# Kernel tuning notes

Hardware: AMD Instinct MI355X
Metric: run time of the kernel (lower is better)

The kernel has to match this reference:

```python
import jax, jax.numpy as jnp
import numpy as np

T = 200                      # TRAIN_ROIS_PER_IMAGE
RATIO = 0.33                 # ROI_POSITIVE_RATIO
P_MAX = int(T * RATIO)       # max positive ROIs (66)
MH, MW = 28, 28              # MASK_SHAPE
STD = jnp.array([0.1, 0.1, 0.2, 0.2], jnp.float32)  # BBOX_STD_DEV
EPS = 1e-6


def _iou(a, b):
    # a [N,4], b [G,4] -> [N,G] IoU (same math as overlaps_graph, without tiling)
    ay1, ax1, ay2, ax2 = a[:, 0:1], a[:, 1:2], a[:, 2:3], a[:, 3:4]
    by1, bx1, by2, bx2 = b[None, :, 0], b[None, :, 1], b[None, :, 2], b[None, :, 3]
    iy = jnp.maximum(jnp.minimum(ay2, by2) - jnp.maximum(ay1, by1), 0.0)
    ix = jnp.maximum(jnp.minimum(ax2, bx2) - jnp.maximum(ax1, bx1), 0.0)
    inter = iy * ix
    union = (ay2 - ay1) * (ax2 - ax1) + (by2 - by1) * (bx2 - bx1) - inter
    return inter / jnp.maximum(union, EPS)


def _box_refinement(box, gt):
    # standard Mask R-CNN box_refinement_graph
    h = jnp.maximum(box[:, 2] - box[:, 0], EPS)
    w = jnp.maximum(box[:, 3] - box[:, 1], EPS)
    cy = box[:, 0] + 0.5 * h
    cx = box[:, 1] + 0.5 * w
    gh = jnp.maximum(gt[:, 2] - gt[:, 0], EPS)
    gw = jnp.maximum(gt[:, 3] - gt[:, 1], EPS)
    gcy = gt[:, 0] + 0.5 * gh
    gcx = gt[:, 1] + 0.5 * gw
    return jnp.stack([(gcy - cy) / h, (gcx - cx) / w,
                      jnp.log(gh / h), jnp.log(gw / w)], axis=-1)


def _crop_and_resize(imgs, boxes):
    # imgs [T,H,W], boxes [T,4] normalized; TF crop_and_resize bilinear semantics,
    # extrapolation_value = 0 for samples outside [0, H-1] x [0, W-1].
    Tn, H, W = imgs.shape
    y1, x1, y2, x2 = boxes[:, 0], boxes[:, 1], boxes[:, 2], boxes[:, 3]
    iy = jnp.arange(MH, dtype=jnp.float32)
    ix = jnp.arange(MW, dtype=jnp.float32)
    ys = y1[:, None] * (H - 1) + iy[None, :] * ((y2 - y1) * (H - 1) / (MH - 1))[:, None]  # [T,MH]
    xs = x1[:, None] * (W - 1) + ix[None, :] * ((x2 - x1) * (W - 1) / (MW - 1))[:, None]  # [T,MW]
    y0 = jnp.floor(ys); x0 = jnp.floor(xs)
    wy = (ys - y0)[:, :, None]
    wx = (xs - x0)[:, None, :]
    y0i = jnp.clip(y0, 0, H - 1).astype(jnp.int32)
    y1i = jnp.clip(y0 + 1, 0, H - 1).astype(jnp.int32)
    x0i = jnp.clip(x0, 0, W - 1).astype(jnp.int32)
    x1i = jnp.clip(x0 + 1, 0, W - 1).astype(jnp.int32)
    t = jnp.arange(Tn)[:, None, None]
    v00 = imgs[t, y0i[:, :, None], x0i[:, None, :]]
    v01 = imgs[t, y0i[:, :, None], x1i[:, None, :]]
    v10 = imgs[t, y1i[:, :, None], x0i[:, None, :]]
    v11 = imgs[t, y1i[:, :, None], x1i[:, None, :]]
    val = (v00 * (1 - wx) + v01 * wx) * (1 - wy) + (v10 * (1 - wx) + v11 * wx) * wy
    ok = ((ys >= 0) & (ys <= H - 1))[:, :, None] & ((xs >= 0) & (xs <= W - 1))[:, None, :]
    return jnp.where(ok, val, 0.0)


def _targets_one(proposals, class_ids, boxes, masks):
    # proposals [N,4], class_ids [G] int, boxes [G,4], masks [H,W,G]
    N = proposals.shape[0]
    # zero-padding trim expressed as validity masks (jit-friendly fixed shapes)
    valid_prop = jnp.any(proposals != 0, axis=1)
    valid_gt = jnp.any(boxes != 0, axis=1)
    non_crowd = (class_ids > 0) & valid_gt
    crowd = (class_ids < 0) & valid_gt

    ov = _iou(proposals, boxes)                              # [N,G]
    ov_nc = jnp.where(non_crowd[None, :], ov, -1.0)          # mask crowd/padded gt
    roi_iou_max = ov_nc.max(axis=1)
    crowd_max = jnp.where(crowd[None, :], ov, 0.0).max(axis=1)

    pos_mask = valid_prop & (roi_iou_max >= 0.5)
    neg_mask = valid_prop & (roi_iou_max < 0.5) & (crowd_max < 0.001)

    # deterministic selection (original uses tf.random.shuffle): positives first-in-order
    pos_order = jnp.argsort(jnp.where(pos_mask, 0, 1))
    neg_order = jnp.argsort(jnp.where(neg_mask, 0, 1))
    pos_count = jnp.minimum(pos_mask.sum(), P_MAX)
    neg_needed = jnp.floor(pos_count.astype(jnp.float32) / RATIO).astype(jnp.int32) - pos_count
    neg_count = jnp.minimum(jnp.minimum(neg_needed, neg_mask.sum()), T - pos_count)

    slot = jnp.arange(T)
    is_pos = slot < pos_count
    is_neg = (slot >= pos_count) & (slot < pos_count + neg_count)
    src = jnp.where(is_pos,
                    pos_order[jnp.clip(slot, 0, N - 1)],
                    neg_order[jnp.clip(slot - pos_count, 0, N - 1)])
    rois = jnp.where((is_pos | is_neg)[:, None], proposals[src], 0.0)

    assign = jnp.argmax(ov_nc[src], axis=1)                  # gt assignment per slot
    gt_box = boxes[assign]
    gt_cls = jnp.where(is_pos, class_ids[assign], 0)

    deltas = _box_refinement(rois, gt_box) / STD
    deltas = jnp.where(is_pos[:, None], deltas, 0.0)

    # USE_MINI_MASK: roi box in gt-box-normalized coordinates
    gy1, gx1, gy2, gx2 = gt_box[:, 0], gt_box[:, 1], gt_box[:, 2], gt_box[:, 3]
    gh = jnp.maximum(gy2 - gy1, EPS)
    gw = jnp.maximum(gx2 - gx1, EPS)
    mm = jnp.stack([(rois[:, 0] - gy1) / gh, (rois[:, 1] - gx1) / gw,
                    (rois[:, 2] - gy1) / gh, (rois[:, 3] - gx1) / gw], axis=-1)

    roi_masks = jnp.moveaxis(jnp.take(masks, assign, axis=2), 2, 0)  # [T,H,W]
    m = jnp.round(_crop_and_resize(roi_masks, mm))
    m = jnp.where(is_pos[:, None, None], m, 0.0)
    return rois, gt_cls, deltas, m


def setup_inputs() -> dict:
    key = jax.random.key(0)
    ks = jax.random.split(key, 4)
    B, N, G, HM = 16, 2000, 200, 56

    def boxes_of(k, shape):
        k1, k2, k3, k4 = jax.random.split(k, 4)
        y1 = jax.random.uniform(k1, shape) * 0.5
        x1 = jax.random.uniform(k2, shape) * 0.5
        h = 0.1 + jax.random.uniform(k3, shape) * 0.4
        w = 0.1 + jax.random.uniform(k4, shape) * 0.4
        return jnp.stack([y1, x1, y1 + h, x1 + w], axis=-1)

    proposals = boxes_of(ks[0], (B, N))
    proposals = proposals * (jnp.arange(N) < N - 200)[None, :, None]  # zero-padded tail
    prior_class_ids = jax.random.randint(ks[1], (B, G), -1, 81).astype(jnp.int32)  # -1=crowd, 0=padding
    prior_boxes = boxes_of(ks[2], (B, G)) * (prior_class_ids != 0)[..., None]
    prior_masks = (jax.random.uniform(ks[3], (B, HM, HM, G)) > 0.5).astype(jnp.float32)
    return {"proposals": proposals, "prior_class_ids": prior_class_ids,
            "prior_boxes": prior_boxes, "prior_masks": prior_masks}


def reference(proposals, prior_class_ids, prior_boxes, prior_masks):
    rois, cls, deltas, masks = jax.vmap(_targets_one)(proposals, prior_class_ids,
                                                      prior_boxes, prior_masks)
    return rois, cls, deltas, masks
```

## Files before the change

### kernel.cpp

```cpp
#include <hip/hip_runtime.h>
#include <math.h>

#pragma clang fp contract(off)

#define BN    16
#define NP    2000
#define NG    200
#define NT    200
#define PMAX  66
#define EPSF  1e-6f
#define MH    28
#define MW    28
#define HM    56
#define NPIX  (HM*HM)
#define NW    49
#define NGP   256
#define NPW   32

#define KA_BLOCKS 128
#define KG_BLOCKS (49*4*BN)

__global__ __launch_bounds__(256) void kF(
    const float* __restrict__ proposals, const int* __restrict__ cls_ids,
    const float* __restrict__ boxes, const float* __restrict__ masks,
    unsigned long long* __restrict__ selbits, int* __restrict__ assign_ws,
    unsigned long long* __restrict__ bits)
{
#pragma clang fp contract(off)
  const int tid  = threadIdx.x;
  const int lane = tid & 63;
  const int wv   = tid >> 6;

  __shared__ float4 gbox[NG];
  __shared__ float  garea[NG];
  __shared__ int    gflag[NG];
  __shared__ unsigned long long sw[64];

  if (blockIdx.x < KA_BLOCKS) {
    const int b = blockIdx.x >> 3;
    const int bxa = blockIdx.x & 7;

    for (int j = tid; j < NG; j += 256) {
      float4 g = reinterpret_cast<const float4*>(boxes + (size_t)b * NG * 4)[j];
      int c = cls_ids[b * NG + j];
      bool vg = (g.x != 0.f) || (g.y != 0.f) || (g.z != 0.f) || (g.w != 0.f);
      gbox[j]  = g;
      garea[j] = (g.z - g.x) * (g.w - g.y);
      gflag[j] = vg ? (c > 0 ? 1 : (c < 0 ? 2 : 0)) : 0;
    }
    __syncthreads();

    const int i  = bxa * 256 + tid;
    const bool act = (i < NP);
    const int ic = act ? i : (NP - 1);

    float4 p = reinterpret_cast<const float4*>(proposals + (size_t)b * NP * 4)[ic];
    bool vp = act && ((p.x != 0.f) || (p.y != 0.f) || (p.z != 0.f) || (p.w != 0.f));
    float pa = (p.z - p.x) * (p.w - p.y);

    float best = -3.0e38f;
    int   bestj = 0;
    float cmax = 0.f;
    for (int j = 0; j < NG; ++j) {
      float4 g = gbox[j];
      float iy = fmaxf(fminf(p.z, g.z) - fmaxf(p.x, g.x), 0.f);
      float ix = fmaxf(fminf(p.w, g.w) - fmaxf(p.y, g.y), 0.f);
      float inter = iy * ix;
      float uni = (pa + garea[j]) - inter;
      float iou = inter / fmaxf(uni, EPSF);
      int fl = gflag[j];
      float v = (fl == 1) ? iou : -1.0f;
      if (v > best) { best = v; bestj = j; }
      if (fl == 2) cmax = fmaxf(cmax, iou);
    }
    bool pos = vp && (best >= 0.5f);
    bool neg = vp && (best < 0.5f) && (cmax < 0.001f);
    unsigned long long bp = __ballot(pos);
    unsigned long long bn = __ballot(neg);
    if (lane == 0) {
      int w = bxa * 4 + wv;
      selbits[(size_t)b * 64 + w]       = bp;
      selbits[(size_t)b * 64 + 32 + w]  = bn;
    }
    if (act) assign_ws[b * NP + i] = bestj;
  } else {
    int idx = blockIdx.x - KA_BLOCKS;
    const int pword = idx % 49;
    idx /= 49;
    const int gw0 = (idx & 3) * 64;
    const int b   = idx >> 2;
    const int p0  = pword * 64;

    const bool gok = (gw0 + lane) < NG;
    const float* mbase = masks + (size_t)b * NPIX * NG + gw0 + lane;
    for (int e = 0; e < 16; ++e) {
      int pl = e * 4 + wv;
      float v = 0.f;
      if (gok) v = mbase[(size_t)(p0 + pl) * NG];
      unsigned long long word = __ballot(v != 0.f);
      if (lane == 0) sw[pl] = word;
    }
    __syncthreads();

    unsigned long long w0 = sw[lane];
    for (int k = 0; k < 16; ++k) {
      int gl = wv * 16 + k;
      unsigned long long word = __ballot((int)((w0 >> gl) & 1ULL));
      if (lane == 0 && (gw0 + gl) < NG)
        bits[(size_t)(b * NGP + gw0 + gl) * NW + pword] = word;
    }
  }
}

__global__ __launch_bounds__(256) void kS(
    const float* __restrict__ proposals, const int* __restrict__ cls_ids,
    const float* __restrict__ boxes, const int* __restrict__ assign_ws,
    const unsigned long long* __restrict__ selbits,
    const unsigned long long* __restrict__ bits, float* __restrict__ out)
{
#pragma clang fp contract(off)
  const int s = blockIdx.x;
  const int b = s / NT;
  const int t = s - b * NT;
  const int q = threadIdx.x;

  __shared__ unsigned long long sel[64];
  __shared__ unsigned long long pb[NW];

  if (q < 64) sel[q] = selbits[(size_t)b * 64 + q];
  __syncthreads();

  int pos_total = 0, neg_total = 0;
  for (int w = 0; w < NPW; ++w) {
    pos_total += __popcll(sel[w]);
    neg_total += __popcll(sel[32 + w]);
  }
  int pos_count = min(pos_total, PMAX);
  int neg_needed = (int)floorf((float)pos_count / 0.33f) - pos_count;
  int neg_count = min(min(neg_needed, neg_total), NT - pos_count);

  const bool ispos = (t < pos_count);
  const bool isneg = (!ispos) && (t < pos_count + neg_count);

  float r0 = 0.f, r1 = 0.f, r2 = 0.f, r3 = 0.f;
  float d0 = 0.f, d1 = 0.f, d2 = 0.f, d3 = 0.f;
  float m0 = 0.f, m1 = 0.f, m2 = 0.f, m3 = 0.f;
  float clsf = 0.f;
  int a = -1;

  if (ispos || isneg) {
    int k = ispos ? t : (t - pos_count);
    const int base = ispos ? 0 : 32;
    int i = 0;
    for (int w = 0; w < NPW; ++w) {
      unsigned long long word = sel[base + w];
      int c = __popcll(word);
      if (k < c) {
        for (int r = 0; r < k; ++r) word &= word - 1ULL;
        i = w * 64 + __builtin_ctzll(word);
        break;
      }
      k -= c;
    }
    float4 p = reinterpret_cast<const float4*>(proposals + (size_t)b * NP * 4)[i];
    r0 = p.x; r1 = p.y; r2 = p.z; r3 = p.w;
    if (ispos) {
      a = assign_ws[b * NP + i];
      float4 g = reinterpret_cast<const float4*>(boxes + (size_t)b * NG * 4)[a];
      float h  = fmaxf(r2 - r0, EPSF);
      float w  = fmaxf(r3 - r1, EPSF);
      float cy = r0 + 0.5f * h;
      float cx = r1 + 0.5f * w;
      float gh = fmaxf(g.z - g.x, EPSF);
      float gw = fmaxf(g.w - g.y, EPSF);
      float gcy = g.x + 0.5f * gh;
      float gcx = g.y + 0.5f * gw;
      d0 = ((gcy - cy) / h) / 0.1f;
      d1 = ((gcx - cx) / w) / 0.1f;
      d2 = logf(gh / h) / 0.2f;
      d3 = logf(gw / w) / 0.2f;
      m0 = (r0 - g.x) / gh;
      m1 = (r1 - g.y) / gw;
      m2 = (r2 - g.x) / gh;
      m3 = (r3 - g.y) / gw;
      clsf = (float)cls_ids[b * NG + a];
    }
  }

  if (q == 0) {
    float* rois = out;
    float* cls  = out + BN * NT * 4;
    float* dlt  = out + BN * NT * 4 + BN * NT;
    rois[s * 4 + 0] = r0; rois[s * 4 + 1] = r1;
    rois[s * 4 + 2] = r2; rois[s * 4 + 3] = r3;
    cls[s] = clsf;
    dlt[s * 4 + 0] = d0; dlt[s * 4 + 1] = d1;
    dlt[s * 4 + 2] = d2; dlt[s * 4 + 3] = d3;
  }

  float4* om = reinterpret_cast<float4*>(
      out + (size_t)(BN * NT * 9) + (size_t)s * (MH * MW));
  if (!ispos) {
    if (q < (MH * MW) / 4) om[q] = make_float4(0.f, 0.f, 0.f, 0.f);
    return;
  }

  if (q < NW) pb[q] = bits[(size_t)(b * NGP + a) * NW + q];
  __syncthreads();
  if (q >= (MH * MW) / 4) return;

  float sy = (m2 - m0) * 55.0f / 27.0f;
  float sx = (m3 - m1) * 55.0f / 27.0f;

  int px0 = q * 4;
  int my  = px0 / MW;
  float ys = m0 * 55.0f + (float)my * sy;
  float y0f = floorf(ys);
  float wy  = ys - y0f;
  int y0i = (int)fminf(fmaxf(y0f, 0.f), 55.f);
  int y1i = (int)fminf(fmaxf(y0f + 1.0f, 0.f), 55.f);
  bool oky = (ys >= 0.f) && (ys <= 55.f);
  const int r0b = y0i * HM;
  const int r1b = y1i * HM;

  float res[4];
  for (int k = 0; k < 4; ++k) {
    int mx = (px0 + k) - my * MW;
    float xs = m1 * 55.0f + (float)mx * sx;
    float x0f = floorf(xs);
    float wx  = xs - x0f;
    int x0i = (int)fminf(fmaxf(x0f, 0.f), 55.f);
    int x1i = (int)fminf(fmaxf(x0f + 1.0f, 0.f), 55.f);
    int p00 = r0b + x0i, p01 = r0b + x1i;
    int p10 = r1b + x0i, p11 = r1b + x1i;
    float v00 = (float)((pb[p00 >> 6] >> (p00 & 63)) & 1ULL);
    float v01 = (float)((pb[p01 >> 6] >> (p01 & 63)) & 1ULL);
    float v10 = (float)((pb[p10 >> 6] >> (p10 & 63)) & 1ULL);
    float v11 = (float)((pb[p11 >> 6] >> (p11 & 63)) & 1ULL);
    float val = (v00 * (1.f - wx) + v01 * wx) * (1.f - wy)
              + (v10 * (1.f - wx) + v11 * wx) * wy;
    bool ok = oky && (xs >= 0.f) && (xs <= 55.f);
    res[k] = ok ? rintf(val) : 0.f;
  }
  om[q] = make_float4(res[0], res[1], res[2], res[3]);
}

extern "C" void kernel_launch(void* const* d_in, const int* in_sizes, int n_in,
                              void* d_out, int out_size, void* d_ws, size_t ws_size,
                              hipStream_t stream)
{
  const float* proposals = (const float*)d_in[0];
  const int*   cls_ids   = (const int*)d_in[1];
  const float* boxes     = (const float*)d_in[2];
  const float* masks     = (const float*)d_in[3];
  float* out = (float*)d_out;

  char* ws = (char*)d_ws;
  unsigned long long* selbits = (unsigned long long*)ws;
  ws += (size_t)BN * 64 * sizeof(unsigned long long);
  unsigned long long* bits_ws = (unsigned long long*)ws;
  ws += (size_t)BN * NGP * NW * sizeof(unsigned long long);
  int* assign_ws = (int*)ws;

  kF<<<KA_BLOCKS + KG_BLOCKS, 256, 0, stream>>>(
      proposals, cls_ids, boxes, masks, selbits, assign_ws, bits_ws);
  kS<<<BN * NT, 256, 0, stream>>>(proposals, cls_ids, boxes, assign_ws,
                                  selbits, bits_ws, out);
}
```

Baseline: 116.0 us.

## Split sampling into per-image ROI kernel and per-ROI mask kernel

```diff
diff --git a/kernel.cpp b/kernel.cpp
--- a/kernel.cpp
+++ b/kernel.cpp
@@ -112,22 +112,18 @@
   }
 }
 
-__global__ __launch_bounds__(256) void kS(
+__global__ __launch_bounds__(256) void kB2(
     const float* __restrict__ proposals, const int* __restrict__ cls_ids,
     const float* __restrict__ boxes, const int* __restrict__ assign_ws,
-    const unsigned long long* __restrict__ selbits,
-    const unsigned long long* __restrict__ bits, float* __restrict__ out)
-{
-#pragma clang fp contract(off)
-  const int s = blockIdx.x;
-  const int b = s / NT;
-  const int t = s - b * NT;
-  const int q = threadIdx.x;
+    const unsigned long long* __restrict__ selbits, float* __restrict__ out,
+    float* __restrict__ mm_ws, int* __restrict__ ma_ws)
+{
+#pragma clang fp contract(off)
+  const int b = blockIdx.x;
+  const int tid = threadIdx.x;
 
   __shared__ unsigned long long sel[64];
-  __shared__ unsigned long long pb[NW];
-
-  if (q < 64) sel[q] = selbits[(size_t)b * 64 + q];
+  if (tid < 64) sel[tid] = selbits[(size_t)b * 64 + tid];
   __syncthreads();
 
   int pos_total = 0, neg_total = 0;
@@ -139,55 +135,57 @@
   int neg_needed = (int)floorf((float)pos_count / 0.33f) - pos_count;
   int neg_count = min(min(neg_needed, neg_total), NT - pos_count);
 
-  const bool ispos = (t < pos_count);
-  const bool isneg = (!ispos) && (t < pos_count + neg_count);
-
-  float r0 = 0.f, r1 = 0.f, r2 = 0.f, r3 = 0.f;
-  float d0 = 0.f, d1 = 0.f, d2 = 0.f, d3 = 0.f;
-  float m0 = 0.f, m1 = 0.f, m2 = 0.f, m3 = 0.f;
-  float clsf = 0.f;
-  int a = -1;
-
-  if (ispos || isneg) {
-    int k = ispos ? t : (t - pos_count);
-    const int base = ispos ? 0 : 32;
-    int i = 0;
-    for (int w = 0; w < NPW; ++w) {
-      unsigned long long word = sel[base + w];
-      int c = __popcll(word);
-      if (k < c) {
-        for (int r = 0; r < k; ++r) word &= word - 1ULL;
-        i = w * 64 + __builtin_ctzll(word);
-        break;
+  if (tid < NT) {
+    const int t = tid;
+    const bool ispos = (t < pos_count);
+    const bool isneg = (!ispos) && (t < pos_count + neg_count);
+
+    float r0 = 0.f, r1 = 0.f, r2 = 0.f, r3 = 0.f;
+    float d0 = 0.f, d1 = 0.f, d2 = 0.f, d3 = 0.f;
+    float m0 = 0.f, m1 = 0.f, m2 = 0.f, m3 = 0.f;
+    float clsf = 0.f;
+    int ma = -1;
+
+    if (ispos || isneg) {
+      int k = ispos ? t : (t - pos_count);
+      const int base = ispos ? 0 : 32;
+      int i = 0;
+      for (int w = 0; w < NPW; ++w) {
+        unsigned long long word = sel[base + w];
+        int c = __popcll(word);
+        if (k < c) {
+          for (int r = 0; r < k; ++r) word &= word - 1ULL;
+          i = w * 64 + __builtin_ctzll(word);
+          break;
+        }
+        k -= c;
       }
-      k -= c;
-    }
-    float4 p = reinterpret_cast<const float4*>(proposals + (size_t)b * NP * 4)[i];
-    r0 = p.x; r1 = p.y; r2 = p.z; r3 = p.w;
-    if (ispos) {
-      a = assign_ws[b * NP + i];
-      float4 g = reinterpret_cast<const float4*>(boxes + (size_t)b * NG * 4)[a];
-      float h  = fmaxf(r2 - r0, EPSF);
-      float w  = fmaxf(r3 - r1, EPSF);
-      float cy = r0 + 0.5f * h;
-      float cx = r1 + 0.5f * w;
-      float gh = fmaxf(g.z - g.x, EPSF);
-      float gw = fmaxf(g.w - g.y, EPSF);
-      float gcy = g.x + 0.5f * gh;
-      float gcx = g.y + 0.5f * gw;
-      d0 = ((gcy - cy) / h) / 0.1f;
-      d1 = ((gcx - cx) / w) / 0.1f;
-      d2 = logf(gh / h) / 0.2f;
-      d3 = logf(gw / w) / 0.2f;
-      m0 = (r0 - g.x) / gh;
-      m1 = (r1 - g.y) / gw;
-      m2 = (r2 - g.x) / gh;
-      m3 = (r3 - g.y) / gw;
-      clsf = (float)cls_ids[b * NG + a];
-    }
-  }
-
-  if (q == 0) {
+      float4 p = reinterpret_cast<const float4*>(proposals + (size_t)b * NP * 4)[i];
+      r0 = p.x; r1 = p.y; r2 = p.z; r3 = p.w;
+      if (ispos) {
+        int a = assign_ws[b * NP + i];
+        ma = a;
+        float4 g = reinterpret_cast<const float4*>(boxes + (size_t)b * NG * 4)[a];
+        float h  = fmaxf(r2 - r0, EPSF);
+        float w  = fmaxf(r3 - r1, EPSF);
+        float cy = r0 + 0.5f * h;
+        float cx = r1 + 0.5f * w;
+        float gh = fmaxf(g.z - g.x, EPSF);
+        float gw = fmaxf(g.w - g.y, EPSF);
+        float gcy = g.x + 0.5f * gh;
+        float gcx = g.y + 0.5f * gw;
+        d0 = ((gcy - cy) / h) / 0.1f;
+        d1 = ((gcx - cx) / w) / 0.1f;
+        d2 = logf(gh / h) / 0.2f;
+        d3 = logf(gw / w) / 0.2f;
+        m0 = (r0 - g.x) / gh;
+        m1 = (r1 - g.y) / gw;
+        m2 = (r2 - g.x) / gh;
+        m3 = (r3 - g.y) / gw;
+        clsf = (float)cls_ids[b * NG + a];
+      }
+    }
+    int s = b * NT + tid;
     float* rois = out;
     float* cls  = out + BN * NT * 4;
     float* dlt  = out + BN * NT * 4 + BN * NT;
@@ -196,25 +194,41 @@
     cls[s] = clsf;
     dlt[s * 4 + 0] = d0; dlt[s * 4 + 1] = d1;
     dlt[s * 4 + 2] = d2; dlt[s * 4 + 3] = d3;
-  }
-
+    mm_ws[s * 4 + 0] = m0; mm_ws[s * 4 + 1] = m1;
+    mm_ws[s * 4 + 2] = m2; mm_ws[s * 4 + 3] = m3;
+    ma_ws[s] = ma;
+  }
+}
+
+__global__ __launch_bounds__(256) void kC(
+    const unsigned long long* __restrict__ bits, const float* __restrict__ mm_ws,
+    const int* __restrict__ ma_ws, float* __restrict__ out)
+{
+#pragma clang fp contract(off)
+  const int s = blockIdx.x;
   float4* om = reinterpret_cast<float4*>(
       out + (size_t)(BN * NT * 9) + (size_t)s * (MH * MW));
-  if (!ispos) {
+  const int q = threadIdx.x;
+  const int a = ma_ws[s];
+  if (a < 0) {
     if (q < (MH * MW) / 4) om[q] = make_float4(0.f, 0.f, 0.f, 0.f);
     return;
   }
 
+  __shared__ unsigned long long pb[NW];
+  const int b = s / NT;
   if (q < NW) pb[q] = bits[(size_t)(b * NGP + a) * NW + q];
   __syncthreads();
   if (q >= (MH * MW) / 4) return;
 
-  float sy = (m2 - m0) * 55.0f / 27.0f;
-  float sx = (m3 - m1) * 55.0f / 27.0f;
+  float y1 = mm_ws[s * 4 + 0], x1 = mm_ws[s * 4 + 1];
+  float y2 = mm_ws[s * 4 + 2], x2 = mm_ws[s * 4 + 3];
+  float sy = (y2 - y1) * 55.0f / 27.0f;
+  float sx = (x2 - x1) * 55.0f / 27.0f;
 
   int px0 = q * 4;
   int my  = px0 / MW;
-  float ys = m0 * 55.0f + (float)my * sy;
+  float ys = y1 * 55.0f + (float)my * sy;
   float y0f = floorf(ys);
   float wy  = ys - y0f;
   int y0i = (int)fminf(fmaxf(y0f, 0.f), 55.f);
@@ -226,7 +240,7 @@
   float res[4];
   for (int k = 0; k < 4; ++k) {
     int mx = (px0 + k) - my * MW;
-    float xs = m1 * 55.0f + (float)mx * sx;
+    float xs = x1 * 55.0f + (float)mx * sx;
     float x0f = floorf(xs);
     float wx  = xs - x0f;
     int x0i = (int)fminf(fmaxf(x0f, 0.f), 55.f);
@@ -261,9 +275,14 @@
   unsigned long long* bits_ws = (unsigned long long*)ws;
   ws += (size_t)BN * NGP * NW * sizeof(unsigned long long);
   int* assign_ws = (int*)ws;
+  ws += (size_t)BN * NP * sizeof(int);
+  float* mm_ws = (float*)ws;
+  ws += (size_t)BN * NT * 4 * sizeof(float);
+  int* ma_ws = (int*)ws;
 
   kF<<<KA_BLOCKS + KG_BLOCKS, 256, 0, stream>>>(
       proposals, cls_ids, boxes, masks, selbits, assign_ws, bits_ws);
-  kS<<<BN * NT, 256, 0, stream>>>(proposals, cls_ids, boxes, assign_ws,
-                                  selbits, bits_ws, out);
-}
+  kB2<<<BN, 256, 0, stream>>>(proposals, cls_ids, boxes, assign_ws, selbits,
+                              out, mm_ws, ma_ws);
+  kC<<<BN * NT, 256, 0, stream>>>(bits_ws, mm_ws, ma_ws, out);
+}
```

Result: no change. 113.8 us (-1.9%).
